# Kernel optimization log

Measured on AMD Instinct MI355X. Metric: run time of the kernel, lower is better.

Reference implementation:

```python
import jax, jax.numpy as jnp
import numpy as np

V, P = 50000, 50
WE, PE = 300, 100
LH = 800            # bidirectional total hidden
H = LH // 2         # per-direction hidden = 400
MH = 1024           # mlp_hidden_dim
B, T = 32, 128


def setup_inputs() -> dict:
    key = jax.random.key(0)
    ks = jax.random.split(key, 16)
    s = 0.05
    inp = {
        "word_tensor": jax.random.randint(ks[0], (B, T), 0, V, dtype=jnp.int32),
        "word_lengths": jnp.full((B,), T, dtype=jnp.int32),
        "pos_tensor": jax.random.randint(ks[1], (B, T), 0, P, dtype=jnp.int32),
        "word_emb": jax.random.normal(ks[2], (V, WE), jnp.float32) * s,
        "pos_emb": jax.random.normal(ks[3], (P, PE), jnp.float32) * s,
        # LSTM layer 0: input dim WE+PE=400; stacked over 2 directions
        "Wih0": jax.random.normal(ks[4], (2, 4 * H, WE + PE), jnp.float32) * s,
        "Whh0": jax.random.normal(ks[5], (2, 4 * H, H), jnp.float32) * s,
        "b0": jnp.zeros((2, 4 * H), jnp.float32),
        # LSTM layer 1: input dim = 2*H = 800
        "Wih1": jax.random.normal(ks[6], (2, 4 * H, LH), jnp.float32) * s,
        "Whh1": jax.random.normal(ks[7], (2, 4 * H, H), jnp.float32) * s,
        "b1": jnp.zeros((2, 4 * H), jnp.float32),
        "Wh": jax.random.normal(ks[8], (MH // 2, LH), jnp.float32) * s,
        "bh": jnp.zeros((MH // 2,), jnp.float32),
        "Wm": jax.random.normal(ks[9], (MH // 2, LH), jnp.float32) * s,
        "bm": jnp.zeros((MH // 2,), jnp.float32),
        "Wo": jax.random.normal(ks[10], (1, MH), jnp.float32) * s,
        "bo": jnp.zeros((1,), jnp.float32),
    }
    return inp


def _lstm_dir(x_tbd, W_ih, W_hh, bias, reverse):
    # x_tbd: [T,B,D]; PyTorch gate order i,f,g,o
    Bsz = x_tbd.shape[1]
    Hd = W_hh.shape[1]
    def cell(carry, xt):
        h, c = carry
        g = xt @ W_ih.T + h @ W_hh.T + bias
        i, f, gg, o = jnp.split(g, 4, axis=-1)
        c = jax.nn.sigmoid(f) * c + jax.nn.sigmoid(i) * jnp.tanh(gg)
        h = jax.nn.sigmoid(o) * jnp.tanh(c)
        return (h, c), h
    init = (jnp.zeros((Bsz, Hd), x_tbd.dtype), jnp.zeros((Bsz, Hd), x_tbd.dtype))
    _, hs = jax.lax.scan(cell, init, x_tbd, reverse=reverse)
    return hs  # [T,B,H], in original time order


def _bilstm_layer(x_btd, Wih, Whh, b):
    x_tbd = jnp.swapaxes(x_btd, 0, 1)
    fwd = _lstm_dir(x_tbd, Wih[0], Whh[0], b[0], reverse=False)
    bwd = _lstm_dir(x_tbd, Wih[1], Whh[1], b[1], reverse=True)
    out = jnp.concatenate([fwd, bwd], axis=-1)  # [T,B,2H]
    return jnp.swapaxes(out, 0, 1)              # [B,T,2H]


def reference(word_tensor, word_lengths, pos_tensor, word_emb, pos_emb,
              Wih0, Whh0, b0, Wih1, Whh1, b1,
              Wh, bh, Wm, bm, Wo, bo):
    embeds = jnp.concatenate([word_emb[word_tensor], pos_emb[pos_tensor]], axis=2)  # [B,T,400]
    h1 = _bilstm_layer(embeds, Wih0, Whh0, b0)   # [B,T,800]
    lstm_out = _bilstm_layer(h1, Wih1, Whh1, b1)  # [B,T,800]
    head_f = lstm_out @ Wh.T + bh   # [B,T,512]
    modif_f = lstm_out @ Wm.T + bm  # [B,T,512]
    # score[b,h,m] = Wo @ tanh(cat(head_f[b,h], modif_f[b,m])) + bo
    # tanh(cat(a,b)) = cat(tanh(a), tanh(b)) -> exact decomposition
    half = Wo.shape[1] // 2
    s_h = jnp.tanh(head_f) @ Wo[0, :half]   # [B,T]
    s_m = jnp.tanh(modif_f) @ Wo[0, half:]  # [B,T]
    score = s_h[:, :, None] + s_m[:, None, :] + bo[0]  # [B,T,T]
    return score
```

## Files before the change

### kernel.cpp

```cpp
#include <hip/hip_runtime.h>

#define DEV __device__ __forceinline__

typedef _Float16 f16;
typedef _Float16 f16x8 __attribute__((ext_vector_type(8)));
typedef float f32x4 __attribute__((ext_vector_type(4)));
typedef unsigned long long ull;

static constexpr int K0P  = 416;
static constexpr int NBLK = 13;
static constexpr int GN   = 3328;
static constexpr int WKP  = 424;
static constexpr int SMEM_LSTM = 128 * WKP * 2;
static constexpr int HB1_ELEM  = 2 * 128 * 13 * 1024;
static constexpr int HB_BYTES  = 2 * HB1_ELEM * 2;
static constexpr unsigned READY0 = 0x80008000u;

DEV float sigf(float x) { return 1.f / (1.f + __expf(-x)); }
DEV float tanhf_(float x) {
  x = fminf(10.f, fmaxf(-10.f, x));
  float e = __expf(2.f * x);
  return (e - 1.f) / (e + 1.f);
}
DEV ull  AL8(const ull* p) { return __hip_atomic_load(p, __ATOMIC_RELAXED, __HIP_MEMORY_SCOPE_AGENT); }
DEV void AS4(unsigned* p, unsigned v) { __hip_atomic_store(p, v, __ATOMIC_RELAXED, __HIP_MEMORY_SCOPE_AGENT); }


__global__ void embed_k(const int* __restrict__ wt, const int* __restrict__ pt,
                        const float* __restrict__ we, const float* __restrict__ pe,
                        f16* __restrict__ x0)
{
  const int r = blockIdx.x;
  const int tid = threadIdx.x;
  const int w = wt[r], p = pt[r];
  const float* wrow = we + (size_t)w * 300;
  const float* prow = pe + (size_t)p * 100;
  f16* xr = x0 + (size_t)r * K0P;
  for (int k = tid; k < K0P; k += 128) {
    float v = (k < 300) ? wrow[k] : (k < 400 ? prow[k - 300] : 0.f);
    xr[k] = (f16)v;
  }
}

__global__ void convpad_k(const float* __restrict__ src, f16* __restrict__ dst,
                          int rows, int K, int KP)
{
  const size_t total = (size_t)rows * KP;
  for (size_t i = (size_t)blockIdx.x * blockDim.x + threadIdx.x; i < total;
       i += (size_t)gridDim.x * blockDim.x) {
    int r = (int)(i / KP), k = (int)(i % KP);
    dst[i] = (f16)(k < K ? src[(size_t)r * K + k] : 0.f);
  }
}

__global__ void wih_reorder_k(const float* __restrict__ src, const float* __restrict__ bias,
                              f16* __restrict__ dst, float* __restrict__ biasr,
                              int K, int KP)
{
  const size_t total = (size_t)GN * KP;
  for (size_t i = (size_t)blockIdx.x * blockDim.x + threadIdx.x; i < total;
       i += (size_t)gridDim.x * blockDim.x) {
    int k = (int)(i % KP);
    int R = (int)(i / KP);
    int d = R / 1664, rr = R % 1664, blk = rr >> 7, loc = rr & 127;
    int w = loc >> 5, t = (loc >> 4) & 1, fq = (loc >> 2) & 3, g = loc & 3;
    int u = blk * 32 + w * 8 + 2 * fq + t;
    float v = (u < 400 && k < K) ? src[((size_t)d * 1600 + g * 400 + u) * K + k] : 0.f;
    dst[i] = (f16)v;
    if (k == 0) biasr[R] = (u < 400) ? bias[d * 1600 + g * 400 + u] : 0.f;
  }
}

__global__ void whh_reorder_k(const float* __restrict__ src, f16* __restrict__ dst)
{
  const int total = 2 * NBLK * 128 * WKP;
  for (int i = blockIdx.x * blockDim.x + threadIdx.x; i < total;
       i += gridDim.x * blockDim.x) {
    int k = i % WKP, loc = (i / WKP) & 127, blk = (i / (WKP * 128)) % NBLK,
        d = i / (WKP * 128 * NBLK);
    int w = loc >> 5, t = (loc >> 4) & 1, fq = (loc >> 2) & 3, g = loc & 3;
    int u = blk * 32 + w * 8 + 2 * fq + t;
    float v = (u < 400 && k < 400) ? src[((size_t)d * 1600 + g * 400 + u) * 400 + k] : 0.f;
    dst[i] = (f16)v;
  }
}

__global__ void biascat_k(const float* __restrict__ bh, const float* __restrict__ bm,
                          float* __restrict__ bhm)
{
  int i = threadIdx.x;
  bhm[i] = i < 512 ? bh[i] : bm[i - 512];
}

__global__ void init_hb_k(unsigned* __restrict__ p, int n)
{
  for (int i = blockIdx.x * blockDim.x + threadIdx.x; i < n; i += gridDim.x * blockDim.x) {
    int off = i % (13 * 512);
    int blk = off >> 9, win = off & 511;
    bool pad = (blk == 12) && ((win >> 7) & 1);
    p[i] = pad ? READY0 : 0u;
  }
}

__global__ __launch_bounds__(256) void gemm_f16_nt(
    const f16* __restrict__ A, const f16* __restrict__ Bw,
    const float* __restrict__ bias, float* __restrict__ C,
    int M, int N, int KP)
{
  __shared__ __align__(16) f16 As[128][40];
  __shared__ __align__(16) f16 Bs[128][40];
  const int tid = threadIdx.x;
  const int bn = blockIdx.x, bm = blockIdx.y;
  const int lane = tid & 63, wid = tid >> 6;
  const int wr = wid >> 1, wc = wid & 1;
  const int srow = tid >> 1, shalf = tid & 1;
  const f16* Ap = A + (size_t)(bm * 128 + srow) * KP + shalf * 16;
  const f16* Bp = Bw + (size_t)(bn * 128 + srow) * KP + shalf * 16;
  const int fr = lane & 15, fq = lane >> 4;
  f32x4 acc[4][4] = {};
  for (int kt = 0; kt < KP; kt += 32) {
    __syncthreads();
    *(uint4*)&As[srow][shalf * 16]     = *(const uint4*)(Ap + kt);
    *(uint4*)&As[srow][shalf * 16 + 8] = *(const uint4*)(Ap + kt + 8);
    *(uint4*)&Bs[srow][shalf * 16]     = *(const uint4*)(Bp + kt);
    *(uint4*)&Bs[srow][shalf * 16 + 8] = *(const uint4*)(Bp + kt + 8);
    __syncthreads();
    f16x8 af[4], bf[4];
    #pragma unroll
    for (int m = 0; m < 4; ++m) af[m] = *(const f16x8*)&As[wr * 64 + m * 16 + fr][fq * 8];
    #pragma unroll
    for (int n = 0; n < 4; ++n) bf[n] = *(const f16x8*)&Bs[wc * 64 + n * 16 + fr][fq * 8];
    #pragma unroll
    for (int m = 0; m < 4; ++m)
      #pragma unroll
      for (int n = 0; n < 4; ++n)
        acc[m][n] = __builtin_amdgcn_mfma_f32_16x16x32_f16(af[m], bf[n], acc[m][n], 0, 0, 0);
  }
  #pragma unroll
  for (int n = 0; n < 4; ++n) {
    const int gn = bn * 128 + wc * 64 + n * 16 + fr;
    const float bv = bias ? bias[gn] : 0.f;
    #pragma unroll
    for (int m = 0; m < 4; ++m) {
      const size_t gm = (size_t)bm * 128 + wr * 64 + m * 16 + fq * 4;
      #pragma unroll
      for (int r = 0; r < 4; ++r)
        C[(gm + r) * (size_t)N + gn] = acc[m][n][r] + bv;
    }
  }
}

__global__ __launch_bounds__(256) void lstm_mfma_k(
    const float* __restrict__ gates,
    const f16* __restrict__ whh_r,
    f16* __restrict__ h_out,
    f16* __restrict__ hB)
{
  extern __shared__ __align__(16) char smem[];
  f16* W_lds = (f16*)smem;

  const int d = blockIdx.x / NBLK, blk = blockIdx.x % NBLK;
  const int tid = threadIdx.x;
  const int lane = tid & 63, w = tid >> 6;
  const int fr = lane & 15, fq = lane >> 4;

  {
    const uint4* src = (const uint4*)(whh_r + ((size_t)d * NBLK + blk) * 128 * WKP);
    uint4* dst = (uint4*)W_lds;
    for (int i = tid; i < 128 * WKP / 8; i += 256) dst[i] = src[i];
  }
  __syncthreads();

  const int u0 = blk * 32 + w * 8 + 2 * fq;
  const bool ok = u0 < 400;
  const float* gbase0 = gates + (size_t)(fr * 128) * GN + d * 1664 + blk * 128 + w * 32;
  const float* gbase1 = gbase0 + (size_t)16 * 128 * GN;
  f16* hout0 = h_out + (size_t)(fr * 128) * 800 + d * 400;
  f16* hout1 = hout0 + (size_t)16 * 128 * 800;
  const f16* a0base = W_lds + (size_t)(w * 32 + fr) * WKP + fq * 8;
  const f16* a1base = a0base + 16 * WKP;
  f16* hb_d = hB + (size_t)d * 128 * 13 * 1024;

  float c00 = 0.f, c01 = 0.f, c10 = 0.f, c11 = 0.f;

  for (int s = 0; s < 128; ++s) {
    const int t = d ? 127 - s : s;
    const float* g0 = gbase0 + (size_t)t * GN;
    const float* g1 = gbase1 + (size_t)t * GN;
    float4 p00 = *(const float4*)(g0 + fq * 4);
    float4 p10 = *(const float4*)(g0 + 16 + fq * 4);
    float4 p01 = *(const float4*)(g1 + fq * 4);
    float4 p11 = *(const float4*)(g1 + 16 + fq * 4);

    f32x4 acc00 = {}, acc01 = {}, acc10 = {}, acc11 = {};
    if (s > 0) {
      const ull* hbq = (const ull*)(hb_d + (size_t)(s - 1) * 13 * 1024) + lane * 2;
      ull q[13][4];
      ull mask = ~0ull;
      for (;;) {
        #pragma unroll
        for (int kk = 0; kk < 13; ++kk) {
          const ull* pp = hbq + kk * 256;
          if ((mask >> (kk * 4 + 0)) & 1) q[kk][0] = AL8(pp);
          if ((mask >> (kk * 4 + 1)) & 1) q[kk][1] = AL8(pp + 1);
          if ((mask >> (kk * 4 + 2)) & 1) q[kk][2] = AL8(pp + 128);
          if ((mask >> (kk * 4 + 3)) & 1) q[kk][3] = AL8(pp + 129);
        }
        __builtin_amdgcn_sched_barrier(0);
        ull nm = 0;
        #pragma unroll
        for (int kk = 0; kk < 13; ++kk)
          #pragma unroll
          for (int j = 0; j < 4; ++j) {
            ull v = q[kk][j];
            if ((unsigned)v == 0u || (unsigned)(v >> 32) == 0u)
              nm |= 1ull << (kk * 4 + j);
          }
        mask = nm;
        if (!__any(nm != 0ull)) break;
        __builtin_amdgcn_s_sleep(1);
      }
      #pragma unroll
      for (int kk = 0; kk < 13; ++kk) {
        f16x8 a0 = *(const f16x8*)(a0base + kk * 32);
        f16x8 a1 = *(const f16x8*)(a1base + kk * 32);
        union { ull u[2]; f16x8 v; } B0, B1;
        B0.u[0] = q[kk][0]; B0.u[1] = q[kk][1];
        B1.u[0] = q[kk][2]; B1.u[1] = q[kk][3];
        acc00 = __builtin_amdgcn_mfma_f32_16x16x32_f16(a0, B0.v, acc00, 0, 0, 0);
        acc01 = __builtin_amdgcn_mfma_f32_16x16x32_f16(a0, B1.v, acc01, 0, 0, 0);
        acc10 = __builtin_amdgcn_mfma_f32_16x16x32_f16(a1, B0.v, acc10, 0, 0, 0);
        acc11 = __builtin_amdgcn_mfma_f32_16x16x32_f16(a1, B1.v, acc11, 0, 0, 0);
      }
    }

    auto act = [&](const f32x4& a, const float4& p, float& c) -> f16 {
      float vi = a[0] + p.x, vf = a[1] + p.y, vg = a[2] + p.z, vo = a[3] + p.w;
      c = sigf(vf) * c + sigf(vi) * tanhf_(vg);
      return (f16)(sigf(vo) * tanhf_(c));
    };
    f16 h00 = act(acc00, p00, c00);
    f16 h10 = act(acc10, p10, c10);
    f16 h01 = act(acc01, p01, c01);
    f16 h11 = act(acc11, p11, c11);

    if (ok) {
      unsigned pk0 = (unsigned)__builtin_bit_cast(unsigned short, h00) |
                     ((unsigned)__builtin_bit_cast(unsigned short, h10) << 16);
      unsigned pk1 = (unsigned)__builtin_bit_cast(unsigned short, h01) |
                     ((unsigned)__builtin_bit_cast(unsigned short, h11) << 16);
      if (pk0 == 0u) pk0 = READY0;
      if (pk1 == 0u) pk1 = READY0;
      unsigned* hbw = (unsigned*)(hb_d + (size_t)s * 13 * 1024 + blk * 1024
                                  + (w * 16 + fr) * 8) + fq;
      AS4(hbw, pk0);
      AS4(hbw + 256, pk1);
      *(unsigned*)(hout0 + (size_t)t * 800 + u0) = pk0;
      *(unsigned*)(hout1 + (size_t)t * 800 + u0) = pk1;
    }
  }
}

__global__ __launch_bounds__(256) void tail_k(const float* __restrict__ feat,
                                              const float* __restrict__ wo,
                                              float* __restrict__ s_h,
                                              float* __restrict__ s_m)
{
  const int r = blockIdx.x;
  const int tid = threadIdx.x;
  const float* fr = feat + (size_t)r * 1024;
  float sum = 0.f;
  const int n0 = tid * 4;
  #pragma unroll
  for (int j = 0; j < 4; ++j) sum += tanhf_(fr[n0 + j]) * wo[n0 + j];
  #pragma unroll
  for (int off = 32; off > 0; off >>= 1) sum += __shfl_down(sum, off, 64);
  __shared__ float red[4];
  if ((tid & 63) == 0) red[tid >> 6] = sum;
  __syncthreads();
  if (tid == 0)       s_h[r] = red[0] + red[1];
  else if (tid == 64) s_m[r] = red[2] + red[3];
}

__global__ void score_k(const float* __restrict__ s_h, const float* __restrict__ s_m,
                        const float* __restrict__ bo, float* __restrict__ out)
{
  const int bh = blockIdx.x;
  const int m = threadIdx.x;
  out[(size_t)bh * 128 + m] = s_h[bh] + s_m[(bh & ~127) + m] + bo[0];
}

extern "C" void kernel_launch(void* const* d_in, const int* in_sizes, int n_in,
                              void* d_out, int out_size, void* d_ws, size_t ws_size,
                              hipStream_t stream)
{
  const int*   wt   = (const int*)d_in[0];
  const int*   pt   = (const int*)d_in[2];
  const float* we   = (const float*)d_in[3];
  const float* pe   = (const float*)d_in[4];
  const float* Wih0 = (const float*)d_in[5];
  const float* Whh0 = (const float*)d_in[6];
  const float* b0   = (const float*)d_in[7];
  const float* Wih1 = (const float*)d_in[8];
  const float* Whh1 = (const float*)d_in[9];
  const float* b1   = (const float*)d_in[10];
  const float* Wh   = (const float*)d_in[11];
  const float* bh   = (const float*)d_in[12];
  const float* Wm   = (const float*)d_in[13];
  const float* bm   = (const float*)d_in[14];
  const float* Wo   = (const float*)d_in[15];
  const float* bo   = (const float*)d_in[16];
  float* out = (float*)d_out;

  char* p = (char*)d_ws;
  auto alloc = [&](size_t bytes) { char* q = p; p += (bytes + 255) & ~(size_t)255; return q; };
  f16*   x0    = (f16*)alloc((size_t)4096 * K0P * 2);
  f16*   wihr0 = (f16*)alloc((size_t)GN * K0P * 2);
  f16*   wihr1 = (f16*)alloc((size_t)GN * 800 * 2);
  f16*   whhr0 = (f16*)alloc((size_t)2 * NBLK * 128 * WKP * 2);
  f16*   whhr1 = (f16*)alloc((size_t)2 * NBLK * 128 * WKP * 2);
  f16*   whm   = (f16*)alloc((size_t)1024 * 800 * 2);
  float* biasr0= (float*)alloc(GN * 4);
  float* biasr1= (float*)alloc(GN * 4);
  float* bhm   = (float*)alloc(1024 * 4);
  float* sh    = (float*)alloc(4096 * 4);
  float* sm    = (float*)alloc(4096 * 4);
  f16*   h1    = (f16*)alloc((size_t)4096 * 800 * 2);
  f16*   h2    = (f16*)alloc((size_t)4096 * 800 * 2);
  f16*   hB    = (f16*)alloc(HB_BYTES);
  float* gates = (float*)alloc((size_t)4096 * GN * 4);
  float* feat  = (float*)gates;

  static bool attr_set = false;
  if (!attr_set) {
    hipFuncSetAttribute((const void*)lstm_mfma_k,
                        hipFuncAttributeMaxDynamicSharedMemorySize, SMEM_LSTM);
    attr_set = true;
  }

  init_hb_k<<<512, 256, 0, stream>>>((unsigned*)hB, HB_BYTES / 4);
  embed_k<<<4096, 128, 0, stream>>>(wt, pt, we, pe, x0);
  wih_reorder_k<<<1024, 256, 0, stream>>>(Wih0, b0, wihr0, biasr0, 400, K0P);
  wih_reorder_k<<<1024, 256, 0, stream>>>(Wih1, b1, wihr1, biasr1, 800, 800);
  whh_reorder_k<<<1024, 256, 0, stream>>>(Whh0, whhr0);
  whh_reorder_k<<<1024, 256, 0, stream>>>(Whh1, whhr1);
  convpad_k<<<1024, 256, 0, stream>>>(Wh, whm, 512, 800, 800);
  convpad_k<<<1024, 256, 0, stream>>>(Wm, whm + (size_t)512 * 800, 512, 800, 800);
  biascat_k<<<1, 1024, 0, stream>>>(bh, bm, bhm);

  gemm_f16_nt<<<dim3(26, 32), 256, 0, stream>>>(x0, wihr0, biasr0, gates, 4096, GN, K0P);
  lstm_mfma_k<<<26, 256, SMEM_LSTM, stream>>>(gates, whhr0, h1, hB);
  gemm_f16_nt<<<dim3(26, 32), 256, 0, stream>>>(h1, wihr1, biasr1, gates, 4096, GN, 800);
  lstm_mfma_k<<<26, 256, SMEM_LSTM, stream>>>(gates, whhr1, h2, hB + HB1_ELEM);
  gemm_f16_nt<<<dim3(8, 32), 256, 0, stream>>>(h2, whm, bhm, feat, 4096, 1024, 800);
  tail_k<<<4096, 256, 0, stream>>>(feat, Wo, sh, sm);
  score_k<<<4096, 128, 0, stream>>>(sh, sm, bo, out);
}
```

Before: 1.679 ms.

## Split recurrent h polling across waves and share via LDS with per-chunk flags

Before this, each of the four waves in an LSTM block polled all 13 k-chunks of the previous step's hidden state from global memory. Now each wave polls only its own 3–4 chunks, copies them into a shared LDS buffer once they are ready, and sets a bit in a workgroup flag word. All waves then wait for the full flag mask and read their MFMA B operands from LDS. This is meant to cut redundant global atomic polling traffic and register pressure on the latency-critical recurrence. In exchange it adds a __syncthreads per timestep, LDS flag atomics and a gate-prefetch reorder, all of which could lengthen each serial step.

```diff
diff --git a/kernel.cpp b/kernel.cpp
--- a/kernel.cpp
+++ b/kernel.cpp
@@ -11,7 +11,9 @@
 static constexpr int NBLK = 13;
 static constexpr int GN   = 3328;
 static constexpr int WKP  = 424;
-static constexpr int SMEM_LSTM = 128 * WKP * 2;
+static constexpr int HX_OFF = 128 * WKP * 2;
+static constexpr int FL_OFF = HX_OFF + 13 * 2560;
+static constexpr int SMEM_LSTM = FL_OFF + 16;
 static constexpr int HB1_ELEM  = 2 * 128 * 13 * 1024;
 static constexpr int HB_BYTES  = 2 * HB1_ELEM * 2;
 static constexpr unsigned READY0 = 0x80008000u;
@@ -157,7 +159,9 @@
     f16* __restrict__ hB)
 {
   extern __shared__ __align__(16) char smem[];
-  f16* W_lds = (f16*)smem;
+  f16*  W_lds = (f16*)smem;
+  char* hx    = smem + HX_OFF;
+  int*  flags = (int*)(smem + FL_OFF);
 
   const int d = blockIdx.x / NBLK, blk = blockIdx.x % NBLK;
   const int tid = threadIdx.x;
@@ -169,6 +173,7 @@
     uint4* dst = (uint4*)W_lds;
     for (int i = tid; i < 128 * WKP / 8; i += 256) dst[i] = src[i];
   }
+  if (tid < 2) flags[tid] = 0;
   __syncthreads();
 
   const int u0 = blk * 32 + w * 8 + 2 * fq;
@@ -181,58 +186,103 @@
   const f16* a1base = a0base + 16 * WKP;
   f16* hb_d = hB + (size_t)d * 128 * 13 * 1024;
 
+  const int nkk = (w == 0) ? 4 : 3;
+  const int kk0 = (w == 0) ? 0 : 4 + 3 * (w - 1);
+
   float c00 = 0.f, c01 = 0.f, c10 = 0.f, c11 = 0.f;
 
   for (int s = 0; s < 128; ++s) {
     const int t = d ? 127 - s : s;
-    const float* g0 = gbase0 + (size_t)t * GN;
-    const float* g1 = gbase1 + (size_t)t * GN;
-    float4 p00 = *(const float4*)(g0 + fq * 4);
-    float4 p10 = *(const float4*)(g0 + 16 + fq * 4);
-    float4 p01 = *(const float4*)(g1 + fq * 4);
-    float4 p11 = *(const float4*)(g1 + 16 + fq * 4);
-
     f32x4 acc00 = {}, acc01 = {}, acc10 = {}, acc11 = {};
+    float4 p00, p10, p01, p11;
+
     if (s > 0) {
-      const ull* hbq = (const ull*)(hb_d + (size_t)(s - 1) * 13 * 1024) + lane * 2;
-      ull q[13][4];
-      ull mask = ~0ull;
-      for (;;) {
+      const ull* slab = (const ull*)(hb_d + (size_t)(s - 1) * 13 * 1024) + lane * 2;
+      ull q[4][4];
+      const unsigned full = (1u << nkk) - 1;
+      unsigned pend = (nkk == 4) ? 0xFFFFu : 0x0FFFu;
+      unsigned wrote = 0, flagged = 0;
+      int* fw = &flags[s & 1];
+      while (flagged != full) {
         #pragma unroll
-        for (int kk = 0; kk < 13; ++kk) {
-          const ull* pp = hbq + kk * 256;
-          if ((mask >> (kk * 4 + 0)) & 1) q[kk][0] = AL8(pp);
-          if ((mask >> (kk * 4 + 1)) & 1) q[kk][1] = AL8(pp + 1);
-          if ((mask >> (kk * 4 + 2)) & 1) q[kk][2] = AL8(pp + 128);
-          if ((mask >> (kk * 4 + 3)) & 1) q[kk][3] = AL8(pp + 129);
-        }
+        for (int i = 0; i < 4; ++i)
+          if (i < nkk) {
+            const ull* pp = slab + (kk0 + i) * 256;
+            if ((pend >> (i * 4 + 0)) & 1) q[i][0] = AL8(pp);
+            if ((pend >> (i * 4 + 1)) & 1) q[i][1] = AL8(pp + 1);
+            if ((pend >> (i * 4 + 2)) & 1) q[i][2] = AL8(pp + 128);
+            if ((pend >> (i * 4 + 3)) & 1) q[i][3] = AL8(pp + 129);
+          }
         __builtin_amdgcn_sched_barrier(0);
-        ull nm = 0;
         #pragma unroll
-        for (int kk = 0; kk < 13; ++kk)
-          #pragma unroll
-          for (int j = 0; j < 4; ++j) {
-            ull v = q[kk][j];
-            if ((unsigned)v == 0u || (unsigned)(v >> 32) == 0u)
-              nm |= 1ull << (kk * 4 + j);
+        for (int i = 0; i < 4; ++i)
+          if (i < nkk)
+            #pragma unroll
+            for (int j = 0; j < 4; ++j)
+              if ((pend >> (i * 4 + j)) & 1) {
+                ull v = q[i][j];
+                if ((unsigned)v != 0u && (unsigned)(v >> 32) != 0u)
+                  pend &= ~(1u << (i * 4 + j));
+              }
+        #pragma unroll
+        for (int i = 0; i < 4; ++i)
+          if (i < nkk && !((wrote >> i) & 1) && ((pend >> (i * 4)) & 15u) == 0u) {
+            char* hp = hx + (kk0 + i) * 2560 + lane * 40;
+            *(ull*)(hp +  0) = q[i][0];
+            *(ull*)(hp +  8) = q[i][1];
+            *(ull*)(hp + 16) = q[i][2];
+            *(ull*)(hp + 24) = q[i][3];
+            wrote |= 1u << i;
           }
-        mask = nm;
-        if (!__any(nm != 0ull)) break;
+        #pragma unroll
+        for (int i = 0; i < 4; ++i)
+          if (i < nkk && !((flagged >> i) & 1)) {
+            bool done = ((pend >> (i * 4)) & 15u) == 0u;
+            if (__all(done)) {
+              asm volatile("s_waitcnt lgkmcnt(0)" ::: "memory");
+              if (lane == 0)
+                __hip_atomic_fetch_or(fw, 1 << (kk0 + i), __ATOMIC_RELAXED,
+                                      __HIP_MEMORY_SCOPE_WORKGROUP);
+              flagged |= 1u << i;
+            }
+          }
+        if (flagged != full) __builtin_amdgcn_s_sleep(2);
+      }
+      const float* g0 = gbase0 + (size_t)t * GN;
+      const float* g1 = gbase1 + (size_t)t * GN;
+      p00 = *(const float4*)(g0 + fq * 4);
+      p10 = *(const float4*)(g0 + 16 + fq * 4);
+      p01 = *(const float4*)(g1 + fq * 4);
+      p11 = *(const float4*)(g1 + 16 + fq * 4);
+      while ((__hip_atomic_load(fw, __ATOMIC_ACQUIRE, __HIP_MEMORY_SCOPE_WORKGROUP)
+              & 0x1FFF) != 0x1FFF)
         __builtin_amdgcn_s_sleep(1);
-      }
+      __builtin_amdgcn_sched_barrier(0);
       #pragma unroll
       for (int kk = 0; kk < 13; ++kk) {
+        const char* hp = hx + kk * 2560 + lane * 40;
         f16x8 a0 = *(const f16x8*)(a0base + kk * 32);
         f16x8 a1 = *(const f16x8*)(a1base + kk * 32);
         union { ull u[2]; f16x8 v; } B0, B1;
-        B0.u[0] = q[kk][0]; B0.u[1] = q[kk][1];
-        B1.u[0] = q[kk][2]; B1.u[1] = q[kk][3];
+        B0.u[0] = *(const ull*)(hp);      B0.u[1] = *(const ull*)(hp + 8);
+        B1.u[0] = *(const ull*)(hp + 16); B1.u[1] = *(const ull*)(hp + 24);
         acc00 = __builtin_amdgcn_mfma_f32_16x16x32_f16(a0, B0.v, acc00, 0, 0, 0);
         acc01 = __builtin_amdgcn_mfma_f32_16x16x32_f16(a0, B1.v, acc01, 0, 0, 0);
         acc10 = __builtin_amdgcn_mfma_f32_16x16x32_f16(a1, B0.v, acc10, 0, 0, 0);
         acc11 = __builtin_amdgcn_mfma_f32_16x16x32_f16(a1, B1.v, acc11, 0, 0, 0);
       }
+    } else {
+      const float* g0 = gbase0 + (size_t)t * GN;
+      const float* g1 = gbase1 + (size_t)t * GN;
+      p00 = *(const float4*)(g0 + fq * 4);
+      p10 = *(const float4*)(g0 + 16 + fq * 4);
+      p01 = *(const float4*)(g1 + fq * 4);
+      p11 = *(const float4*)(g1 + 16 + fq * 4);
     }
+
+    __syncthreads();
+    if (tid == 0)
+      __hip_atomic_store(&flags[s & 1], 0, __ATOMIC_RELAXED, __HIP_MEMORY_SCOPE_WORKGROUP);
 
     auto act = [&](const f32x4& a, const float4& p, float& c) -> f16 {
       float vi = a[0] + p.x, vf = a[1] + p.y, vg = a[2] + p.z, vo = a[3] + p.w;
```

Result: faster. 1.366 ms, median of 2 (-18.6%).
